# Kernel optimization log

Hardware: AMD Instinct MI355X
Metric: run time of the kernel (lower is better)

Reference implementation:

```python
import jax, jax.numpy as jnp
import numpy as np

D = 768      # d_model (BERT-base)
H = 8        # MatTransformer heads
DK = D // H  # 96
L = 4        # MatTransformer layers
FF = 1024    # MatTransformer hidden_size
NREL = 97    # num_relations
BAG = 8      # bag_len (docs per bag)
SEQ = 512    # seq_len
NB = 3       # bridge entities per doc
S = 2 + NB   # spans per doc: h, t, bridges
E = BAG * S  # total entities = 40
NEG = -1e30


def setup_inputs() -> dict:
    key = jax.random.key(0)
    ks = jax.random.split(key, 30)
    w = lambda k, shp: jax.random.normal(k, shp, jnp.float32) * 0.02
    inp = {
        "embedding": jax.random.normal(ks[0], (BAG, SEQ, D), jnp.float32),
        "spans": jnp.sort(jax.random.randint(ks[1], (BAG, S, 2), 0, SEQ, jnp.int32), axis=-1),
        # Codred pairwise-relation params (torch Linear stored as [in, out])
        "wu_w": w(ks[2], (D, D)), "wu_b": jnp.zeros((D,), jnp.float32),
        "wvv_w": w(ks[3], (D, D)), "wvv_b": jnp.zeros((D,), jnp.float32),
        "lnr_w": w(ks[4], (D, D)), "lnr_b": jnp.zeros((D,), jnp.float32),
        # MatTransformer params, stacked over layers
        "matt_wq": w(ks[5], (L, D, D)), "matt_bq": jnp.zeros((L, D), jnp.float32),
        "matt_wk": w(ks[6], (L, D, D)), "matt_bk": jnp.zeros((L, D), jnp.float32),
        "matt_wv": w(ks[7], (L, D, D)), "matt_bv": jnp.zeros((L, D), jnp.float32),
        "matt_wo": w(ks[8], (L, D, D)), "matt_bo": jnp.zeros((L, D), jnp.float32),
        "matt_w1": w(ks[9], (L, D, FF)), "matt_b1": jnp.zeros((L, FF), jnp.float32),
        "matt_w2": w(ks[10], (L, FF, D)), "matt_b2": jnp.zeros((L, D), jnp.float32),
        "matt_g1": jnp.ones((L, D), jnp.float32), "matt_be1": jnp.zeros((L, D), jnp.float32),
        "matt_g2": jnp.ones((L, D), jnp.float32), "matt_be2": jnp.zeros((L, D), jnp.float32),
        # relation predictor
        "pred_w": w(ks[11], (D, NREL)), "pred_b": jnp.zeros((NREL,), jnp.float32),
    }
    return inp


def _layernorm(x, g, b, eps=1e-5):
    m = jnp.mean(x, axis=-1, keepdims=True)
    v = jnp.var(x, axis=-1, keepdims=True)
    return (x - m) * jax.lax.rsqrt(v + eps) * g + b


def reference(embedding, spans, wu_w, wu_b, wvv_w, wvv_b, lnr_w, lnr_b,
              matt_wq, matt_bq, matt_wk, matt_bk, matt_wv, matt_bv, matt_wo, matt_bo,
              matt_w1, matt_b1, matt_w2, matt_b2, matt_g1, matt_be1, matt_g2, matt_be2,
              pred_w, pred_b):
    # --- entity span max-pool (gather + max over inclusive [start, end]) ---
    pos = jnp.arange(SEQ)
    span_mask = (pos[None, None, :] >= spans[..., 0:1]) & (pos[None, None, :] <= spans[..., 1:2])  # [BAG,S,SEQ]
    pooled = jnp.max(jnp.where(span_mask[..., None], embedding[:, None, :, :], NEG), axis=2)  # [BAG,S,D]
    htb = pooled.reshape(E, D)  # per-doc order: h, t, b1..bNB (matches htb_embs stacking)

    # --- pairwise relation matrix: relu(ln1(relu(u_i + v_j))) ---
    u = htb @ wu_w + wu_b                       # [E,D]
    v = htb @ wvv_w + wvv_b                     # [E,D]
    alpha = jax.nn.relu(u[:, None, :] + v[None, :, :])          # [E,E,D]
    rel = jax.nn.relu(alpha @ lnr_w + lnr_b)                    # [E,E,D]

    # --- MatTransformer: encoder over the E*E relation tokens (rel_mask all ones) ---
    T = E * E
    x = rel.reshape(T, D)
    scale = 1.0 / np.sqrt(DK).astype(np.float32)
    for l in range(L):
        q = (x @ matt_wq[l] + matt_bq[l]).reshape(T, H, DK)
        k = (x @ matt_wk[l] + matt_bk[l]).reshape(T, H, DK)
        vv = (x @ matt_wv[l] + matt_bv[l]).reshape(T, H, DK)
        scores = jnp.einsum('thd,shd->hts', q, k) * scale       # [H,T,T]
        attn = jax.nn.softmax(scores, axis=-1)
        o = jnp.einsum('hts,shd->thd', attn, vv).reshape(T, D)
        o = o @ matt_wo[l] + matt_bo[l]
        x = _layernorm(x + o, matt_g1[l], matt_be1[l])
        ff = jax.nn.relu(x @ matt_w1[l] + matt_b1[l]) @ matt_w2[l] + matt_b2[l]
        x = _layernorm(x + ff, matt_g2[l], matt_be2[l])
    rel_m = x.reshape(E, E, D)

    # --- gather (h, t) relation features, predict, bag max-pool over logits ---
    h_pos = jnp.arange(BAG) * S      # head entity index per doc
    t_pos = h_pos + 1                # tail entity index per doc
    ht_feat = rel_m[h_pos, t_pos]    # [BAG,D]
    ht_logits = ht_feat @ pred_w + pred_b          # [BAG,NREL]
    bag_logit = jnp.max(ht_logits, axis=0, keepdims=True)  # [1,NREL]
    return bag_logit
```

## Files before the change

### kernel.cpp

```cpp
#include <hip/hip_runtime.h>


#define D    768
#define H    8
#define DKD  96
#define LAY  4
#define FFD  1024
#define NREL 97
#define BAG  8
#define SPANS 5
#define E    40
#define TT   1600
#define SEQ  512
#define D3   2304
#define NS   3

typedef __attribute__((ext_vector_type(8))) short bf16x8;
typedef __attribute__((ext_vector_type(4))) float f32x4;
typedef unsigned short ushort_t;
typedef unsigned int uint_t;

__device__ __forceinline__ ushort_t f2b(float x) {
    uint_t u = __builtin_bit_cast(uint_t, x);
    return (ushort_t)((u + 0x7fffu + ((u >> 16) & 1u)) >> 16);
}
__device__ __forceinline__ float b2f(ushort_t v) {
    return __builtin_bit_cast(float, (uint_t)v << 16);
}

__device__ __forceinline__ void gload16(const void* g, void* l) {
    __builtin_amdgcn_global_load_lds(
        (const __attribute__((address_space(1))) unsigned int*)g,
        (__attribute__((address_space(3))) unsigned int*)l, 16, 0, 0);
}

__device__ __forceinline__ float block_sum(float v, float* red) {
#pragma unroll
    for (int o = 32; o >= 1; o >>= 1) v += __shfl_xor(v, o);
    __syncthreads();
    if ((threadIdx.x & 63) == 0) red[threadIdx.x >> 6] = v;
    __syncthreads();
    return red[0] + red[1] + red[2] + red[3];
}

__global__ __launch_bounds__(256) void span_pool_p1(const float* __restrict__ emb,
        const int* __restrict__ spans, float* __restrict__ partial) {
    const int e = blockIdx.x, pg = blockIdx.y;
    const int bag = e / SPANS;
    const int st = spans[e * 2 + 0];
    const int en = spans[e * 2 + 1];
    const int p0 = max(st, pg * 64);
    const int p1 = min(en, pg * 64 + 63);
    const int tid = threadIdx.x;
    if (tid >= 192) return;
    float4 m = make_float4(-1e30f, -1e30f, -1e30f, -1e30f);
    for (int p = p0; p <= p1; ++p) {
        const float4 v = *(const float4*)(emb + ((size_t)bag * SEQ + p) * D + tid * 4);
        m.x = fmaxf(m.x, v.x); m.y = fmaxf(m.y, v.y);
        m.z = fmaxf(m.z, v.z); m.w = fmaxf(m.w, v.w);
    }
    *(float4*)(partial + ((size_t)e * 8 + pg) * D + tid * 4) = m;
}

__global__ __launch_bounds__(256) void span_pool_p2(const float* __restrict__ partial,
        float* __restrict__ htb) {
    const int e = blockIdx.x;
    const int tid = threadIdx.x;
    if (tid >= 192) return;
    float4 m = make_float4(-1e30f, -1e30f, -1e30f, -1e30f);
#pragma unroll
    for (int pg = 0; pg < 8; ++pg) {
        const float4 v = *(const float4*)(partial + ((size_t)e * 8 + pg) * D + tid * 4);
        m.x = fmaxf(m.x, v.x); m.y = fmaxf(m.y, v.y);
        m.z = fmaxf(m.z, v.z); m.w = fmaxf(m.w, v.w);
    }
    *(float4*)(htb + (size_t)e * D + tid * 4) = m;
}

__global__ __launch_bounds__(256) void alpha_k(const float* __restrict__ u,
        const float* __restrict__ v, ushort_t* __restrict__ a) {
    const int ij = blockIdx.x;
    const int i = ij / E, j = ij % E;
    const int tid = threadIdx.x;
#pragma unroll
    for (int t2 = 0; t2 < 3; ++t2) {
        const int d = tid + t2 * 256;
        a[(size_t)ij * D + d] = f2b(fmaxf(u[(size_t)i * D + d] + v[(size_t)j * D + d], 0.f));
    }
}

__global__ __launch_bounds__(256) void gemm_uv(const float* __restrict__ A,
        const float* __restrict__ B0, const float* __restrict__ bias0, float* __restrict__ C0,
        const float* __restrict__ B1, const float* __restrict__ bias1, float* __restrict__ C1,
        int M, int N, int K) {
    const float* B = blockIdx.z ? B1 : B0;
    const float* bias = blockIdx.z ? bias1 : bias0;
    float* C = blockIdx.z ? C1 : C0;
    __shared__ float As[16][68];
    __shared__ float Bs[16][68];
    const int bn = blockIdx.x * 64;
    const int bm = blockIdx.y * 64;
    const int tid = threadIdx.x;
    const int tx = tid & 15;
    const int ty = tid >> 4;
    const int ar = tid >> 2;
    const int ac = (tid & 3) << 2;
    const int br = tid >> 4;
    const int bc = (tid & 15) << 2;
    float acc[4][4] = {};
    for (int k0 = 0; k0 < K; k0 += 16) {
        float4 av;
        if (bm + ar < M) av = *(const float4*)(A + (size_t)(bm + ar) * K + k0 + ac);
        else             av = make_float4(0.f, 0.f, 0.f, 0.f);
        const float4 bv = *(const float4*)(B + (size_t)(k0 + br) * N + bn + bc);
        As[ac + 0][ar] = av.x; As[ac + 1][ar] = av.y;
        As[ac + 2][ar] = av.z; As[ac + 3][ar] = av.w;
        *(float4*)&Bs[br][bc] = bv;
        __syncthreads();
#pragma unroll
        for (int kk = 0; kk < 16; ++kk) {
            const float4 a = *(const float4*)&As[kk][ty << 2];
            const float4 b = *(const float4*)&Bs[kk][tx << 2];
            acc[0][0] += a.x * b.x; acc[0][1] += a.x * b.y; acc[0][2] += a.x * b.z; acc[0][3] += a.x * b.w;
            acc[1][0] += a.y * b.x; acc[1][1] += a.y * b.y; acc[1][2] += a.y * b.z; acc[1][3] += a.y * b.w;
            acc[2][0] += a.z * b.x; acc[2][1] += a.z * b.y; acc[2][2] += a.z * b.z; acc[2][3] += a.z * b.w;
            acc[3][0] += a.w * b.x; acc[3][1] += a.w * b.y; acc[3][2] += a.w * b.z; acc[3][3] += a.w * b.w;
        }
        __syncthreads();
    }
#pragma unroll
    for (int i = 0; i < 4; ++i) {
        const int row = bm + (ty << 2) + i;
        if (row >= M) continue;
#pragma unroll
        for (int j = 0; j < 4; ++j) {
            const int col = bn + (tx << 2) + j;
            C[(size_t)row * N + col] = acc[i][j] + bias[col];
        }
    }
}

__global__ __launch_bounds__(256) void transpose_cast(const float* __restrict__ S0,
        const float* __restrict__ S1, const float* __restrict__ S2,
        const float* __restrict__ S3, ushort_t* __restrict__ dst, int K, int N) {
    __shared__ float t[32][33];
    const float* src = (blockIdx.z == 0) ? S0 : (blockIdx.z == 1) ? S1 :
                       (blockIdx.z == 2) ? S2 : S3;
    ushort_t* d = dst + (size_t)blockIdx.z * K * N;
    const int n0 = blockIdx.x * 32, k0 = blockIdx.y * 32;
    const int tx = threadIdx.x & 31, ty = threadIdx.x >> 5;
#pragma unroll
    for (int i = 0; i < 4; ++i)
        t[ty + i * 8][tx] = src[(size_t)(k0 + ty + i * 8) * N + n0 + tx];
    __syncthreads();
#pragma unroll
    for (int i = 0; i < 4; ++i)
        d[(size_t)(n0 + ty + i * 8) * K + k0 + tx] = f2b(t[tx][ty + i * 8]);
}

__global__ __launch_bounds__(256) void concat_bias(const float* __restrict__ bq,
        const float* __restrict__ bk, const float* __restrict__ bv,
        float* __restrict__ dst) {
    const int i = blockIdx.x * 256 + threadIdx.x;
    if (i >= LAY * D3) return;
    const int l = i / D3, j = i % D3;
    float v;
    if (j < D) v = bq[l * D + j];
    else if (j < 2 * D) v = bk[l * D + j - D];
    else v = bv[l * D + j - 2 * D];
    dst[i] = v;
}

template<int RELU>
__global__ __launch_bounds__(256) void gemm_mfma(const ushort_t* __restrict__ A,
        const ushort_t* __restrict__ Bt, const float* __restrict__ bias,
        float* __restrict__ Cf, ushort_t* __restrict__ Cb, int M, int N, int K) {
    __shared__ ushort_t As[128 * 32];
    __shared__ ushort_t Bs[64 * 32];
    const int tid = threadIdx.x;
    const int lane = tid & 63, w = tid >> 6;
    const int l15 = lane & 15, lg = lane >> 4;
    const int bm = blockIdx.y * 128, bn = blockIdx.x * 64;
    const int wm = (w >> 1) * 64, wn = (w & 1) * 32;
    const int trA0 = w * 32 + (lane >> 2);
    const int trA1 = trA0 + 16;
    const int trB  = w * 16 + (lane >> 2);
    const int sc   = (lane & 3) * 8;
    const size_t rowA0 = (size_t)min(bm + trA0, M - 1) * K;
    const size_t rowA1 = (size_t)min(bm + trA1, M - 1) * K;
    const size_t rowB  = (size_t)(bn + trB) * K;
    ushort_t* asd0 = As + w * 1024;
    ushort_t* asd1 = As + w * 1024 + 512;
    ushort_t* bsd  = Bs + w * 512;

    f32x4 acc[4][2];
#pragma unroll
    for (int mi = 0; mi < 4; ++mi)
#pragma unroll
        for (int ni = 0; ni < 2; ++ni)
            acc[mi][ni] = (f32x4){0.f, 0.f, 0.f, 0.f};

    for (int k0 = 0; k0 < K; k0 += 32) {
        __syncthreads();
        gload16(A + rowA0 + k0 + sc, asd0);
        gload16(A + rowA1 + k0 + sc, asd1);
        gload16(Bt + rowB + k0 + sc, bsd);
        __syncthreads();
        bf16x8 af[4], bfr[2];
#pragma unroll
        for (int mi = 0; mi < 4; ++mi)
            af[mi] = *(const bf16x8*)&As[(wm + mi * 16 + l15) * 32 + lg * 8];
#pragma unroll
        for (int ni = 0; ni < 2; ++ni)
            bfr[ni] = *(const bf16x8*)&Bs[(wn + ni * 16 + l15) * 32 + lg * 8];
        __builtin_amdgcn_s_setprio(1);
#pragma unroll
        for (int mi = 0; mi < 4; ++mi)
#pragma unroll
            for (int ni = 0; ni < 2; ++ni)
                acc[mi][ni] = __builtin_amdgcn_mfma_f32_16x16x32_bf16(
                    af[mi], bfr[ni], acc[mi][ni], 0, 0, 0);
        __builtin_amdgcn_s_setprio(0);
    }
#pragma unroll
    for (int mi = 0; mi < 4; ++mi)
#pragma unroll
        for (int ni = 0; ni < 2; ++ni)
#pragma unroll
            for (int r = 0; r < 4; ++r) {
                const int row = bm + wm + mi * 16 + lg * 4 + r;
                if (row >= M) continue;
                const int col = bn + wn + ni * 16 + l15;
                float v = acc[mi][ni][r] + bias[col];
                if (RELU) v = fmaxf(v, 0.f);
                if (Cf) Cf[(size_t)row * N + col] = v;
                if (Cb) Cb[(size_t)row * N + col] = f2b(v);
            }
}

__global__ __launch_bounds__(256) void attn_part(const ushort_t* __restrict__ Q,
        const ushort_t* __restrict__ K, const ushort_t* __restrict__ V,
        ushort_t* __restrict__ Opart, float* __restrict__ ml, int ldin) {
    __shared__ ushort_t Qs[64][104];
    __shared__ ushort_t Ks[64][104];
    __shared__ ushort_t Vt[96][76];
    __shared__ ushort_t Ps[4][16][72];
    const int q0 = blockIdx.x * 64;
    const int h = blockIdx.y;
    const int cch = blockIdx.z;
    const int t_lo = (cch * (TT / 64)) / NS;
    const int t_hi = ((cch + 1) * (TT / 64)) / NS;
    const int tid = threadIdx.x;
    const int lane = tid & 63, w = tid >> 6;
    const int l15 = lane & 15, lg = lane >> 4;
    const float scale = 0.10206207261596577f;

    int r_[3], c_[3];
#pragma unroll
    for (int i = 0; i < 3; ++i) {
        const int ch = i * 256 + tid;
        r_[i] = ch / 12; c_[i] = (ch % 12) * 8;
    }
#pragma unroll
    for (int i = 0; i < 3; ++i) {
        const uint4 v4 = *(const uint4*)(Q + (size_t)(q0 + r_[i]) * ldin + h * DKD + c_[i]);
        *(uint4*)&Qs[r_[i]][c_[i]] = v4;
    }
    uint4 kreg[3], vreg[3];
    {
        const int s0 = t_lo * 64;
#pragma unroll
        for (int i = 0; i < 3; ++i) {
            kreg[i] = *(const uint4*)(K + (size_t)(s0 + r_[i]) * ldin + h * DKD + c_[i]);
            vreg[i] = *(const uint4*)(V + (size_t)(s0 + r_[i]) * ldin + h * DKD + c_[i]);
        }
    }
    float m_run[4], l_run[4];
    f32x4 acc_o[6];
#pragma unroll
    for (int r = 0; r < 4; ++r) { m_run[r] = -1e30f; l_run[r] = 0.f; }
#pragma unroll
    for (int nt = 0; nt < 6; ++nt) acc_o[nt] = (f32x4){0.f, 0.f, 0.f, 0.f};

    for (int t = t_lo; t < t_hi; ++t) {
        __syncthreads();
#pragma unroll
        for (int i = 0; i < 3; ++i) {
            *(uint4*)&Ks[r_[i]][c_[i]] = kreg[i];
            const ushort_t* pv = (const ushort_t*)&vreg[i];
#pragma unroll
            for (int j = 0; j < 8; ++j) Vt[c_[i] + j][r_[i]] = pv[j];
        }
        __syncthreads();
        if (t + 1 < t_hi) {
            const int s0 = (t + 1) * 64;
#pragma unroll
            for (int i = 0; i < 3; ++i) {
                kreg[i] = *(const uint4*)(K + (size_t)(s0 + r_[i]) * ldin + h * DKD + c_[i]);
                vreg[i] = *(const uint4*)(V + (size_t)(s0 + r_[i]) * ldin + h * DKD + c_[i]);
            }
        }
        f32x4 accs[4];
#pragma unroll
        for (int ni = 0; ni < 4; ++ni) accs[ni] = (f32x4){0.f, 0.f, 0.f, 0.f};
        __builtin_amdgcn_s_setprio(1);
#pragma unroll
        for (int ks = 0; ks < 3; ++ks) {
            const bf16x8 aq = *(const bf16x8*)&Qs[w * 16 + l15][ks * 32 + lg * 8];
#pragma unroll
            for (int ni = 0; ni < 4; ++ni) {
                const bf16x8 bk = *(const bf16x8*)&Ks[ni * 16 + l15][ks * 32 + lg * 8];
                accs[ni] = __builtin_amdgcn_mfma_f32_16x16x32_bf16(aq, bk, accs[ni], 0, 0, 0);
            }
        }
        __builtin_amdgcn_s_setprio(0);
        float ps[4][4];
#pragma unroll
        for (int r = 0; r < 4; ++r) {
#pragma unroll
            for (int ni = 0; ni < 4; ++ni) ps[ni][r] = accs[ni][r] * scale;
            float mx = fmaxf(fmaxf(ps[0][r], ps[1][r]), fmaxf(ps[2][r], ps[3][r]));
#pragma unroll
            for (int o = 1; o <= 8; o <<= 1) mx = fmaxf(mx, __shfl_xor(mx, o));
            const float mnew = fmaxf(m_run[r], mx);
            const float sf = __expf(m_run[r] - mnew);
            m_run[r] = mnew;
            float rs = 0.f;
#pragma unroll
            for (int ni = 0; ni < 4; ++ni) {
                ps[ni][r] = __expf(ps[ni][r] - mnew);
                rs += ps[ni][r];
            }
#pragma unroll
            for (int o = 1; o <= 8; o <<= 1) rs += __shfl_xor(rs, o);
            l_run[r] = l_run[r] * sf + rs;
#pragma unroll
            for (int nt = 0; nt < 6; ++nt) acc_o[nt][r] *= sf;
        }
#pragma unroll
        for (int ni = 0; ni < 4; ++ni)
#pragma unroll
            for (int r = 0; r < 4; ++r)
                Ps[w][lg * 4 + r][ni * 16 + l15] = f2b(ps[ni][r]);
        __builtin_amdgcn_s_setprio(1);
#pragma unroll
        for (int ks = 0; ks < 2; ++ks) {
            const bf16x8 ap = *(const bf16x8*)&Ps[w][l15][ks * 32 + lg * 8];
#pragma unroll
            for (int nt = 0; nt < 6; ++nt) {
                const bf16x8 bv = *(const bf16x8*)&Vt[nt * 16 + l15][ks * 32 + lg * 8];
                acc_o[nt] = __builtin_amdgcn_mfma_f32_16x16x32_bf16(ap, bv, acc_o[nt], 0, 0, 0);
            }
        }
        __builtin_amdgcn_s_setprio(0);
    }
#pragma unroll
    for (int nt = 0; nt < 6; ++nt)
#pragma unroll
        for (int r = 0; r < 4; ++r) {
            const int row = q0 + w * 16 + lg * 4 + r;
            const int col = h * DKD + nt * 16 + l15;
            Opart[((size_t)cch * TT + row) * D + col] = f2b(acc_o[nt][r]);
        }
    if (l15 == 0) {
#pragma unroll
        for (int r = 0; r < 4; ++r) {
            const int row = q0 + w * 16 + lg * 4 + r;
            float2* mlp = (float2*)ml;
            mlp[((size_t)cch * H + h) * TT + row] = make_float2(m_run[r], l_run[r]);
        }
    }
}

__global__ __launch_bounds__(256) void attn_combine(const ushort_t* __restrict__ Opart,
        const float* __restrict__ ml, ushort_t* __restrict__ O) {
    const int row = blockIdx.x;
    const int tid = threadIdx.x;
    const float2* mlp = (const float2*)ml;
#pragma unroll
    for (int kk = 0; kk < 3; ++kk) {
        const int col = tid + kk * 256;
        const int h = col / DKD;
        float m[NS], l[NS], M = -1e30f;
#pragma unroll
        for (int c = 0; c < NS; ++c) {
            const float2 v = mlp[((size_t)c * H + h) * TT + row];
            m[c] = v.x; l[c] = v.y; M = fmaxf(M, m[c]);
        }
        float L = 0.f, o = 0.f;
#pragma unroll
        for (int c = 0; c < NS; ++c) {
            const float e = __expf(m[c] - M);
            L += l[c] * e;
            o += b2f(Opart[((size_t)c * TT + row) * D + col]) * e;
        }
        O[(size_t)row * D + col] = f2b(o / L);
    }
}

__global__ __launch_bounds__(256) void add_ln(float* __restrict__ x,
        const float* __restrict__ y, const float* __restrict__ g,
        const float* __restrict__ b, ushort_t* __restrict__ xb) {
    __shared__ float red[4];
    const int row = blockIdx.x;
    const int tid = threadIdx.x;
    float vals[3];
    float s = 0.f;
#pragma unroll
    for (int i = 0; i < 3; ++i) {
        const int c = tid + i * 256;
        const float t = x[(size_t)row * D + c] + y[(size_t)row * D + c];
        vals[i] = t; s += t;
    }
    const float mean = block_sum(s, red) * (1.f / 768.f);
    float s2 = 0.f;
#pragma unroll
    for (int i = 0; i < 3; ++i) { const float dd = vals[i] - mean; s2 += dd * dd; }
    const float var = block_sum(s2, red) * (1.f / 768.f);
    const float inv = rsqrtf(var + 1e-5f);
#pragma unroll
    for (int i = 0; i < 3; ++i) {
        const int c = tid + i * 256;
        const float o = (vals[i] - mean) * inv * g[c] + b[c];
        x[(size_t)row * D + c] = o;
        xb[(size_t)row * D + c] = f2b(o);
    }
}

__global__ __launch_bounds__(256) void predict_k(const float* __restrict__ x,
        const float* __restrict__ pw, const float* __restrict__ pb,
        float* __restrict__ out) {
    __shared__ float red[4];
    const int r = blockIdx.x;
    const int tid = threadIdx.x;
    float best = -1e30f;
    for (int bag = 0; bag < BAG; ++bag) {
        const int row = (bag * SPANS) * E + (bag * SPANS + 1);
        const float* f = x + (size_t)row * D;
        float acc = 0.f;
        for (int d = tid; d < D; d += 256) acc += f[d] * pw[(size_t)d * NREL + r];
        best = fmaxf(best, block_sum(acc, red));
    }
    if (tid == 0) out[r] = best + pb[r];
}

extern "C" void kernel_launch(void* const* d_in, const int* in_sizes, int n_in,
                              void* d_out, int out_size, void* d_ws, size_t ws_size,
                              hipStream_t stream) {
    const float* emb  = (const float*)d_in[0];
    const int*  spans = (const int*)d_in[1];
    const float* wu_w = (const float*)d_in[2];  const float* wu_b = (const float*)d_in[3];
    const float* wvv_w= (const float*)d_in[4];  const float* wvv_b= (const float*)d_in[5];
    const float* lnr_w= (const float*)d_in[6];  const float* lnr_b= (const float*)d_in[7];
    const float* wq = (const float*)d_in[8];    const float* bq = (const float*)d_in[9];
    const float* wk = (const float*)d_in[10];   const float* bk = (const float*)d_in[11];
    const float* wv = (const float*)d_in[12];   const float* bv = (const float*)d_in[13];
    const float* wo = (const float*)d_in[14];   const float* bo = (const float*)d_in[15];
    const float* w1 = (const float*)d_in[16];   const float* b1 = (const float*)d_in[17];
    const float* w2 = (const float*)d_in[18];   const float* b2 = (const float*)d_in[19];
    const float* g1 = (const float*)d_in[20];   const float* be1= (const float*)d_in[21];
    const float* g2 = (const float*)d_in[22];   const float* be2= (const float*)d_in[23];
    const float* pw = (const float*)d_in[24];   const float* pb = (const float*)d_in[25];

    char* cur = (char*)d_ws;
    auto alloc = [&](size_t bytes) { char* p = cur; cur += (bytes + 255) & ~(size_t)255; return p; };
    float*    htb  = (float*)alloc(E * D * 4);
    float*    ub   = (float*)alloc(E * D * 4);
    float*    vb   = (float*)alloc(E * D * 4);
    float*    part = (float*)alloc((size_t)E * 8 * D * 4);
    float*    x    = (float*)alloc((size_t)TT * D * 4);
    ushort_t* xb   = (ushort_t*)alloc((size_t)TT * D * 2);
    ushort_t* qkv  = (ushort_t*)alloc((size_t)TT * D3 * 2);
    ushort_t* ob   = (ushort_t*)alloc((size_t)TT * D * 2);
    float*    tb   = (float*)alloc((size_t)TT * D * 4);
    ushort_t* fb   = (ushort_t*)alloc((size_t)TT * FFD * 2);
    ushort_t* lnrT = (ushort_t*)alloc((size_t)D * D * 2);
    ushort_t* wT4  = (ushort_t*)alloc((size_t)4 * D * D * 2);
    ushort_t* w1T  = (ushort_t*)alloc((size_t)D * FFD * 2);
    ushort_t* w2T  = (ushort_t*)alloc((size_t)FFD * D * 2);
    float*    bqkv = (float*)alloc((size_t)LAY * D3 * 4);
    ushort_t* Opart = (ushort_t*)tb;
    float*    ml    = part;

    const int DD = D * D;

    span_pool_p1<<<dim3(E, 8), 256, 0, stream>>>(emb, spans, part);
    span_pool_p2<<<E, 256, 0, stream>>>(part, htb);
    gemm_uv<<<dim3(D / 64, 1, 2), 256, 0, stream>>>(htb, wu_w, wu_b, ub, wvv_w, wvv_b, vb, E, D, D);
    alpha_k<<<TT, 256, 0, stream>>>(ub, vb, ob);
    transpose_cast<<<dim3(D / 32, D / 32, 1), 256, 0, stream>>>(lnr_w, lnr_w, lnr_w, lnr_w, lnrT, D, D);
    concat_bias<<<(LAY * D3 + 255) / 256, 256, 0, stream>>>(bq, bk, bv, bqkv);
    gemm_mfma<1><<<dim3(D / 64, (TT + 127) / 128), 256, 0, stream>>>(ob, lnrT, lnr_b, x, xb, TT, D, D);

    for (int l = 0; l < LAY; ++l) {
        transpose_cast<<<dim3(D / 32, D / 32, 4), 256, 0, stream>>>(
            wq + (size_t)l * DD, wk + (size_t)l * DD, wv + (size_t)l * DD, wo + (size_t)l * DD, wT4, D, D);
        transpose_cast<<<dim3(FFD / 32, D / 32, 1), 256, 0, stream>>>(
            w1 + (size_t)l * D * FFD, w1, w1, w1, w1T, D, FFD);
        transpose_cast<<<dim3(D / 32, FFD / 32, 1), 256, 0, stream>>>(
            w2 + (size_t)l * FFD * D, w2, w2, w2, w2T, FFD, D);

        gemm_mfma<0><<<dim3(D3 / 64, (TT + 127) / 128), 256, 0, stream>>>(
            xb, wT4, bqkv + l * D3, nullptr, qkv, TT, D3, D);
        attn_part<<<dim3(TT / 64, H, NS), 256, 0, stream>>>(
            qkv, qkv + D, qkv + 2 * D, Opart, ml, D3);
        attn_combine<<<TT, 256, 0, stream>>>(Opart, ml, ob);
        gemm_mfma<0><<<dim3(D / 64, (TT + 127) / 128), 256, 0, stream>>>(
            ob, wT4 + 3 * DD, bo + l * D, tb, nullptr, TT, D, D);
        add_ln<<<TT, 256, 0, stream>>>(x, tb, g1 + l * D, be1 + l * D, xb);
        gemm_mfma<1><<<dim3(FFD / 64, (TT + 127) / 128), 256, 0, stream>>>(
            xb, w1T, b1 + l * FFD, nullptr, fb, TT, FFD, D);
        gemm_mfma<0><<<dim3(D / 64, (TT + 127) / 128), 256, 0, stream>>>(
            fb, w2T, b2 + l * D, tb, nullptr, TT, D, FFD);
        add_ln<<<TT, 256, 0, stream>>>(x, tb, g2 + l * D, be2 + l * D, xb);
    }

    predict_k<<<NREL, 256, 0, stream>>>(x, pw, pb, (float*)d_out);
    (void)in_sizes; (void)n_in; (void)out_size; (void)ws_size;
}
```

Before: 711.7 us.

## Use double-buffered 128x128 MFMA GEMM everywhere and merge weight transposes

The MFMA GEMM tile grows from 128x64 to 128x128, and its LDS staging is double-buffered so the next K tile loads while the current one computes. The fp32 u/v GEMM is replaced by the bf16 MFMA GEMM over a concatenated [wu|wvv] weight, so the span pool now emits bf16. The per-layer weight transposes are merged into one launch, and the initial lnr/wu/wvv transposes into another, with workspace buffers reused. The goal is fewer launches and better operand reuse, but 128x128 tiles give far fewer blocks for M=1600 (e.g. 78 blocks for the N=768 GEMMs), which risks underfilling the GPU.

```diff
diff --git a/kernel.cpp b/kernel.cpp
--- a/kernel.cpp
+++ b/kernel.cpp
@@ -63,7 +63,7 @@
 }
 
 __global__ __launch_bounds__(256) void span_pool_p2(const float* __restrict__ partial,
-        float* __restrict__ htb) {
+        ushort_t* __restrict__ htb) {
     const int e = blockIdx.x;
     const int tid = threadIdx.x;
     if (tid >= 192) return;
@@ -74,80 +74,61 @@
         m.x = fmaxf(m.x, v.x); m.y = fmaxf(m.y, v.y);
         m.z = fmaxf(m.z, v.z); m.w = fmaxf(m.w, v.w);
     }
-    *(float4*)(htb + (size_t)e * D + tid * 4) = m;
-}
-
-__global__ __launch_bounds__(256) void alpha_k(const float* __restrict__ u,
-        const float* __restrict__ v, ushort_t* __restrict__ a) {
+    ushort4 o;
+    o.x = f2b(m.x); o.y = f2b(m.y); o.z = f2b(m.z); o.w = f2b(m.w);
+    *(ushort4*)(htb + (size_t)e * D + tid * 4) = o;
+}
+
+__global__ __launch_bounds__(256) void alpha_k(const float* __restrict__ uv,
+        ushort_t* __restrict__ a) {
     const int ij = blockIdx.x;
     const int i = ij / E, j = ij % E;
     const int tid = threadIdx.x;
 #pragma unroll
     for (int t2 = 0; t2 < 3; ++t2) {
         const int d = tid + t2 * 256;
-        a[(size_t)ij * D + d] = f2b(fmaxf(u[(size_t)i * D + d] + v[(size_t)j * D + d], 0.f));
-    }
-}
-
-__global__ __launch_bounds__(256) void gemm_uv(const float* __restrict__ A,
-        const float* __restrict__ B0, const float* __restrict__ bias0, float* __restrict__ C0,
-        const float* __restrict__ B1, const float* __restrict__ bias1, float* __restrict__ C1,
-        int M, int N, int K) {
-    const float* B = blockIdx.z ? B1 : B0;
-    const float* bias = blockIdx.z ? bias1 : bias0;
-    float* C = blockIdx.z ? C1 : C0;
-    __shared__ float As[16][68];
-    __shared__ float Bs[16][68];
-    const int bn = blockIdx.x * 64;
-    const int bm = blockIdx.y * 64;
-    const int tid = threadIdx.x;
-    const int tx = tid & 15;
-    const int ty = tid >> 4;
-    const int ar = tid >> 2;
-    const int ac = (tid & 3) << 2;
-    const int br = tid >> 4;
-    const int bc = (tid & 15) << 2;
-    float acc[4][4] = {};
-    for (int k0 = 0; k0 < K; k0 += 16) {
-        float4 av;
-        if (bm + ar < M) av = *(const float4*)(A + (size_t)(bm + ar) * K + k0 + ac);
-        else             av = make_float4(0.f, 0.f, 0.f, 0.f);
-        const float4 bv = *(const float4*)(B + (size_t)(k0 + br) * N + bn + bc);
-        As[ac + 0][ar] = av.x; As[ac + 1][ar] = av.y;
-        As[ac + 2][ar] = av.z; As[ac + 3][ar] = av.w;
-        *(float4*)&Bs[br][bc] = bv;
-        __syncthreads();
-#pragma unroll
-        for (int kk = 0; kk < 16; ++kk) {
-            const float4 a = *(const float4*)&As[kk][ty << 2];
-            const float4 b = *(const float4*)&Bs[kk][tx << 2];
-            acc[0][0] += a.x * b.x; acc[0][1] += a.x * b.y; acc[0][2] += a.x * b.z; acc[0][3] += a.x * b.w;
-            acc[1][0] += a.y * b.x; acc[1][1] += a.y * b.y; acc[1][2] += a.y * b.z; acc[1][3] += a.y * b.w;
-            acc[2][0] += a.z * b.x; acc[2][1] += a.z * b.y; acc[2][2] += a.z * b.z; acc[2][3] += a.z * b.w;
-            acc[3][0] += a.w * b.x; acc[3][1] += a.w * b.y; acc[3][2] += a.w * b.z; acc[3][3] += a.w * b.w;
-        }
-        __syncthreads();
-    }
-#pragma unroll
-    for (int i = 0; i < 4; ++i) {
-        const int row = bm + (ty << 2) + i;
-        if (row >= M) continue;
-#pragma unroll
-        for (int j = 0; j < 4; ++j) {
-            const int col = bn + (tx << 2) + j;
-            C[(size_t)row * N + col] = acc[i][j] + bias[col];
-        }
-    }
-}
-
-__global__ __launch_bounds__(256) void transpose_cast(const float* __restrict__ S0,
-        const float* __restrict__ S1, const float* __restrict__ S2,
-        const float* __restrict__ S3, ushort_t* __restrict__ dst, int K, int N) {
+        a[(size_t)ij * D + d] =
+            f2b(fmaxf(uv[(size_t)i * 1536 + d] + uv[(size_t)j * 1536 + 768 + d], 0.f));
+    }
+}
+
+__global__ __launch_bounds__(256) void transpose_up(const float* __restrict__ lnr,
+        const float* __restrict__ wu, const float* __restrict__ wvv,
+        ushort_t* __restrict__ lnrT, ushort_t* __restrict__ wuvT) {
     __shared__ float t[32][33];
-    const float* src = (blockIdx.z == 0) ? S0 : (blockIdx.z == 1) ? S1 :
-                       (blockIdx.z == 2) ? S2 : S3;
-    ushort_t* d = dst + (size_t)blockIdx.z * K * N;
+    const int z = blockIdx.z;
+    const float* src = (z == 0) ? lnr : (z == 1) ? wu : wvv;
+    ushort_t* dst = (z == 0) ? lnrT : wuvT + (size_t)(z - 1) * D * D;
     const int n0 = blockIdx.x * 32, k0 = blockIdx.y * 32;
+    const int tx = threadIdx.x & 31, ty = threadIdx.x >> 5;
+#pragma unroll
+    for (int i = 0; i < 4; ++i)
+        t[ty + i * 8][tx] = src[(size_t)(k0 + ty + i * 8) * D + n0 + tx];
+    __syncthreads();
+#pragma unroll
+    for (int i = 0; i < 4; ++i)
+        dst[(size_t)(n0 + ty + i * 8) * D + k0 + tx] = f2b(t[tx][ty + i * 8]);
+}
+
+__global__ __launch_bounds__(256) void transpose_layer(const float* __restrict__ wq,
+        const float* __restrict__ wk, const float* __restrict__ wv,
+        const float* __restrict__ wo, const float* __restrict__ w1,
+        const float* __restrict__ w2, int l, ushort_t* __restrict__ wT4,
+        ushort_t* __restrict__ w1T, ushort_t* __restrict__ w2T) {
+    __shared__ float t[32][33];
+    const int z = blockIdx.z;
+    const float* src; ushort_t* dst; int K, N;
+    if (z < 4) {
+        K = D; N = D;
+        src = (z == 0 ? wq : z == 1 ? wk : z == 2 ? wv : wo) + (size_t)l * D * D;
+        dst = wT4 + (size_t)z * D * D;
+    } else if (z == 4) {
+        K = D; N = FFD; src = w1 + (size_t)l * D * FFD; dst = w1T;
+    } else {
+        K = FFD; N = D; src = w2 + (size_t)l * FFD * D; dst = w2T;
+    }
+    const int n0 = blockIdx.x * 32, k0 = blockIdx.y * 32;
+    if (n0 >= N || k0 >= K) return;
     const int tx = threadIdx.x & 31, ty = threadIdx.x >> 5;
 #pragma unroll
     for (int i = 0; i < 4; ++i)
@@ -155,77 +136,82 @@
     __syncthreads();
 #pragma unroll
     for (int i = 0; i < 4; ++i)
-        d[(size_t)(n0 + ty + i * 8) * K + k0 + tx] = f2b(t[tx][ty + i * 8]);
+        dst[(size_t)(n0 + ty + i * 8) * K + k0 + tx] = f2b(t[tx][ty + i * 8]);
 }
 
 __global__ __launch_bounds__(256) void concat_bias(const float* __restrict__ bq,
         const float* __restrict__ bk, const float* __restrict__ bv,
-        float* __restrict__ dst) {
+        const float* __restrict__ bu, const float* __restrict__ bvv,
+        float* __restrict__ bqkv, float* __restrict__ buv) {
     const int i = blockIdx.x * 256 + threadIdx.x;
-    if (i >= LAY * D3) return;
-    const int l = i / D3, j = i % D3;
-    float v;
-    if (j < D) v = bq[l * D + j];
-    else if (j < 2 * D) v = bk[l * D + j - D];
-    else v = bv[l * D + j - 2 * D];
-    dst[i] = v;
+    if (i < LAY * D3) {
+        const int l = i / D3, j = i % D3;
+        bqkv[i] = j < D ? bq[l * D + j] : j < 2 * D ? bk[l * D + j - D] : bv[l * D + j - 2 * D];
+    }
+    const int k = i - LAY * D3;
+    if (k >= 0 && k < 2 * D) buv[k] = k < D ? bu[k] : bvv[k - D];
 }
 
 template<int RELU>
-__global__ __launch_bounds__(256) void gemm_mfma(const ushort_t* __restrict__ A,
+__global__ __launch_bounds__(256) void gemm128(const ushort_t* __restrict__ A,
         const ushort_t* __restrict__ Bt, const float* __restrict__ bias,
         float* __restrict__ Cf, ushort_t* __restrict__ Cb, int M, int N, int K) {
-    __shared__ ushort_t As[128 * 32];
-    __shared__ ushort_t Bs[64 * 32];
+    __shared__ ushort_t As[2][128 * 32];
+    __shared__ ushort_t Bs[2][128 * 32];
     const int tid = threadIdx.x;
     const int lane = tid & 63, w = tid >> 6;
     const int l15 = lane & 15, lg = lane >> 4;
-    const int bm = blockIdx.y * 128, bn = blockIdx.x * 64;
-    const int wm = (w >> 1) * 64, wn = (w & 1) * 32;
-    const int trA0 = w * 32 + (lane >> 2);
-    const int trA1 = trA0 + 16;
-    const int trB  = w * 16 + (lane >> 2);
-    const int sc   = (lane & 3) * 8;
-    const size_t rowA0 = (size_t)min(bm + trA0, M - 1) * K;
-    const size_t rowA1 = (size_t)min(bm + trA1, M - 1) * K;
-    const size_t rowB  = (size_t)(bn + trB) * K;
-    ushort_t* asd0 = As + w * 1024;
-    ushort_t* asd1 = As + w * 1024 + 512;
-    ushort_t* bsd  = Bs + w * 512;
-
-    f32x4 acc[4][2];
+    const int bm = blockIdx.y * 128, bn = blockIdx.x * 128;
+    const int wm = (w >> 1) * 64, wn = (w & 1) * 64;
+    const int srow = lane >> 2;
+    const int scol = (lane & 3) * 8;
+    const int rA0 = w * 32 + srow, rA1 = rA0 + 16;
+    const size_t gA0 = (size_t)min(bm + rA0, M - 1) * K + scol;
+    const size_t gA1 = (size_t)min(bm + rA1, M - 1) * K + scol;
+    const size_t gB0 = (size_t)min(bn + rA0, N - 1) * K + scol;
+    const size_t gB1 = (size_t)min(bn + rA1, N - 1) * K + scol;
+
+    f32x4 acc[4][4];
 #pragma unroll
     for (int mi = 0; mi < 4; ++mi)
 #pragma unroll
-        for (int ni = 0; ni < 2; ++ni)
+        for (int ni = 0; ni < 4; ++ni)
             acc[mi][ni] = (f32x4){0.f, 0.f, 0.f, 0.f};
 
-    for (int k0 = 0; k0 < K; k0 += 32) {
-        __syncthreads();
-        gload16(A + rowA0 + k0 + sc, asd0);
-        gload16(A + rowA1 + k0 + sc, asd1);
-        gload16(Bt + rowB + k0 + sc, bsd);
-        __syncthreads();
-        bf16x8 af[4], bfr[2];
+    auto STAGE = [&](int buf, int k0) {
+        gload16(A + gA0 + k0, &As[buf][w * 1024]);
+        gload16(A + gA1 + k0, &As[buf][w * 1024 + 512]);
+        gload16(Bt + gB0 + k0, &Bs[buf][w * 1024]);
+        gload16(Bt + gB1 + k0, &Bs[buf][w * 1024 + 512]);
+    };
+
+    const int nt = K / 32;
+    STAGE(0, 0);
+    __syncthreads();
+    for (int t = 0; t < nt; ++t) {
+        const int buf = t & 1;
+        if (t + 1 < nt) STAGE(buf ^ 1, (t + 1) * 32);
+        bf16x8 af[4], bfr[4];
 #pragma unroll
         for (int mi = 0; mi < 4; ++mi)
-            af[mi] = *(const bf16x8*)&As[(wm + mi * 16 + l15) * 32 + lg * 8];
-#pragma unroll
-        for (int ni = 0; ni < 2; ++ni)
-            bfr[ni] = *(const bf16x8*)&Bs[(wn + ni * 16 + l15) * 32 + lg * 8];
+            af[mi] = *(const bf16x8*)&As[buf][(wm + mi * 16 + l15) * 32 + lg * 8];
+#pragma unroll
+        for (int ni = 0; ni < 4; ++ni)
+            bfr[ni] = *(const bf16x8*)&Bs[buf][(wn + ni * 16 + l15) * 32 + lg * 8];
         __builtin_amdgcn_s_setprio(1);
 #pragma unroll
         for (int mi = 0; mi < 4; ++mi)
 #pragma unroll
-            for (int ni = 0; ni < 2; ++ni)
+            for (int ni = 0; ni < 4; ++ni)
                 acc[mi][ni] = __builtin_amdgcn_mfma_f32_16x16x32_bf16(
                     af[mi], bfr[ni], acc[mi][ni], 0, 0, 0);
         __builtin_amdgcn_s_setprio(0);
+        __syncthreads();
     }
 #pragma unroll
     for (int mi = 0; mi < 4; ++mi)
 #pragma unroll
-        for (int ni = 0; ni < 2; ++ni)
+        for (int ni = 0; ni < 4; ++ni)
 #pragma unroll
             for (int r = 0; r < 4; ++r) {
                 const int row = bm + wm + mi * 16 + lg * 4 + r;
@@ -464,9 +450,8 @@
 
     char* cur = (char*)d_ws;
     auto alloc = [&](size_t bytes) { char* p = cur; cur += (bytes + 255) & ~(size_t)255; return p; };
-    float*    htb  = (float*)alloc(E * D * 4);
-    float*    ub   = (float*)alloc(E * D * 4);
-    float*    vb   = (float*)alloc(E * D * 4);
+    ushort_t* htb  = (ushort_t*)alloc(E * D * 2);
+    float*    uvb  = (float*)alloc((size_t)E * 1536 * 4);
     float*    part = (float*)alloc((size_t)E * 8 * D * 4);
     float*    x    = (float*)alloc((size_t)TT * D * 4);
     ushort_t* xb   = (ushort_t*)alloc((size_t)TT * D * 2);
@@ -474,43 +459,39 @@
     ushort_t* ob   = (ushort_t*)alloc((size_t)TT * D * 2);
     float*    tb   = (float*)alloc((size_t)TT * D * 4);
     ushort_t* fb   = (ushort_t*)alloc((size_t)TT * FFD * 2);
-    ushort_t* lnrT = (ushort_t*)alloc((size_t)D * D * 2);
     ushort_t* wT4  = (ushort_t*)alloc((size_t)4 * D * D * 2);
     ushort_t* w1T  = (ushort_t*)alloc((size_t)D * FFD * 2);
     ushort_t* w2T  = (ushort_t*)alloc((size_t)FFD * D * 2);
     float*    bqkv = (float*)alloc((size_t)LAY * D3 * 4);
+    float*    buv  = (float*)alloc((size_t)2 * D * 4);
     ushort_t* Opart = (ushort_t*)tb;
     float*    ml    = part;
+    ushort_t* wuvT  = wT4;
+    ushort_t* lnrT  = w1T;
 
     const int DD = D * D;
 
     span_pool_p1<<<dim3(E, 8), 256, 0, stream>>>(emb, spans, part);
     span_pool_p2<<<E, 256, 0, stream>>>(part, htb);
-    gemm_uv<<<dim3(D / 64, 1, 2), 256, 0, stream>>>(htb, wu_w, wu_b, ub, wvv_w, wvv_b, vb, E, D, D);
-    alpha_k<<<TT, 256, 0, stream>>>(ub, vb, ob);
-    transpose_cast<<<dim3(D / 32, D / 32, 1), 256, 0, stream>>>(lnr_w, lnr_w, lnr_w, lnr_w, lnrT, D, D);
-    concat_bias<<<(LAY * D3 + 255) / 256, 256, 0, stream>>>(bq, bk, bv, bqkv);
-    gemm_mfma<1><<<dim3(D / 64, (TT + 127) / 128), 256, 0, stream>>>(ob, lnrT, lnr_b, x, xb, TT, D, D);
+    transpose_up<<<dim3(24, 24, 3), 256, 0, stream>>>(lnr_w, wu_w, wvv_w, lnrT, wuvT);
+    concat_bias<<<(LAY * D3 + 2 * D + 255) / 256, 256, 0, stream>>>(bq, bk, bv, wu_b, wvv_b, bqkv, buv);
+    gemm128<0><<<dim3(1536 / 128, 1), 256, 0, stream>>>(htb, wuvT, buv, uvb, nullptr, E, 1536, D);
+    alpha_k<<<TT, 256, 0, stream>>>(uvb, ob);
+    gemm128<1><<<dim3(D / 128, (TT + 127) / 128), 256, 0, stream>>>(ob, lnrT, lnr_b, x, xb, TT, D, D);
 
     for (int l = 0; l < LAY; ++l) {
-        transpose_cast<<<dim3(D / 32, D / 32, 4), 256, 0, stream>>>(
-            wq + (size_t)l * DD, wk + (size_t)l * DD, wv + (size_t)l * DD, wo + (size_t)l * DD, wT4, D, D);
-        transpose_cast<<<dim3(FFD / 32, D / 32, 1), 256, 0, stream>>>(
-            w1 + (size_t)l * D * FFD, w1, w1, w1, w1T, D, FFD);
-        transpose_cast<<<dim3(D / 32, FFD / 32, 1), 256, 0, stream>>>(
-            w2 + (size_t)l * FFD * D, w2, w2, w2, w2T, FFD, D);
-
-        gemm_mfma<0><<<dim3(D3 / 64, (TT + 127) / 128), 256, 0, stream>>>(
+        transpose_layer<<<dim3(32, 32, 6), 256, 0, stream>>>(wq, wk, wv, wo, w1, w2, l, wT4, w1T, w2T);
+        gemm128<0><<<dim3(D3 / 128, (TT + 127) / 128), 256, 0, stream>>>(
             xb, wT4, bqkv + l * D3, nullptr, qkv, TT, D3, D);
         attn_part<<<dim3(TT / 64, H, NS), 256, 0, stream>>>(
             qkv, qkv + D, qkv + 2 * D, Opart, ml, D3);
         attn_combine<<<TT, 256, 0, stream>>>(Opart, ml, ob);
-        gemm_mfma<0><<<dim3(D / 64, (TT + 127) / 128), 256, 0, stream>>>(
+        gemm128<0><<<dim3(D / 128, (TT + 127) / 128), 256, 0, stream>>>(
             ob, wT4 + 3 * DD, bo + l * D, tb, nullptr, TT, D, D);
         add_ln<<<TT, 256, 0, stream>>>(x, tb, g1 + l * D, be1 + l * D, xb);
-        gemm_mfma<1><<<dim3(FFD / 64, (TT + 127) / 128), 256, 0, stream>>>(
+        gemm128<1><<<dim3(FFD / 128, (TT + 127) / 128), 256, 0, stream>>>(
             xb, w1T, b1 + l * FFD, nullptr, fb, TT, FFD, D);
-        gemm_mfma<0><<<dim3(D / 64, (TT + 127) / 128), 256, 0, stream>>>(
+        gemm128<0><<<dim3(D / 128, (TT + 127) / 128), 256, 0, stream>>>(
             fb, w2T, b2 + l * D, tb, nullptr, TT, D, FFD);
         add_ln<<<TT, 256, 0, stream>>>(x, tb, g2 + l * D, be2 + l * D, xb);
     }
```

Measured after the change: 800.0 us. 12.4% more time.
